# Performance work log

Hardware: AMD Instinct MI355X
Metric: run time of the kernel (lower is better)

## Reference

```python
import jax, jax.numpy as jnp
import numpy as np
from functools import partial

S, N, G2, R, E, IN, OUT = 32, 400, 16, 128, 64, 2, 5


def setup_inputs() -> dict:
    key = jax.random.key(0)
    ks = jax.random.split(key, 16)
    sc = lambda *sh: 1.0 / np.sqrt(sh[-1] if len(sh) > 1 else sh[0])
    return {
        "input_data": jax.random.normal(ks[0], (S, N, IN), jnp.float32),
        "grids": jax.random.uniform(ks[1], (S, N, N, G2), jnp.float32) * (jax.random.uniform(ks[2], (S, N, N, G2)) < 0.05),  # mostly-sparse grid masks
        "hidden_states": jax.random.normal(ks[3], (N, R), jnp.float32) * 0.1,
        "cell_states": jax.random.normal(ks[4], (N, R), jnp.float32) * 0.1,
        "W_in": jax.random.normal(ks[5], (IN, E), jnp.float32) * 0.5,
        "b_in": jax.random.normal(ks[6], (E,), jnp.float32) * 0.1,
        "W_t": jax.random.normal(ks[7], (G2 * R, E), jnp.float32) / np.sqrt(G2 * R),
        "b_t": jax.random.normal(ks[8], (E,), jnp.float32) * 0.1,
        "W_ih": jax.random.normal(ks[9], (4 * R, 2 * E), jnp.float32) / np.sqrt(2 * E),
        "b_ih": jax.random.normal(ks[10], (4 * R,), jnp.float32) * 0.1,
        "W_hh": jax.random.normal(ks[11], (4 * R, R), jnp.float32) / np.sqrt(R),
        "b_hh": jax.random.normal(ks[12], (4 * R,), jnp.float32) * 0.1,
        "W_out": jax.random.normal(ks[13], (R, OUT), jnp.float32) / np.sqrt(R),
        "b_out": jax.random.normal(ks[14], (OUT,), jnp.float32) * 0.1,
    }


def reference(input_data, grids, hidden_states, cell_states, W_in, b_in, W_t, b_t,
              W_ih, b_ih, W_hh, b_hh, W_out, b_out):
    n = hidden_states.shape[0]

    def step(carry, frame):
        h, c = carry
        x_f, grid_f = frame  # [N,2], [N,N,G2]
        # social tensor: for each node, grid[node].T @ hidden  -> [N, G2, R]
        social = jnp.einsum('nmg,mr->ngr', grid_f, h).reshape(n, -1)
        input_emb = jax.nn.relu(x_f @ W_in + b_in)          # dropout = identity (eval)
        tensor_emb = jax.nn.relu(social @ W_t + b_t)
        z = jnp.concatenate([input_emb, tensor_emb], axis=1)  # [N, 2E]
        gates = z @ W_ih.T + b_ih + h @ W_hh.T + b_hh         # [N, 4R]
        i, f, g, o = jnp.split(gates, 4, axis=1)              # torch LSTMCell gate order
        c_new = jax.nn.sigmoid(f) * c + jax.nn.sigmoid(i) * jnp.tanh(g)
        h_new = jax.nn.sigmoid(o) * jnp.tanh(c_new)
        out = h_new @ W_out + b_out
        return (h_new, c_new), out

    (h_fin, c_fin), outputs = jax.lax.scan(step, (hidden_states, cell_states), (input_data, grids))
    return outputs, h_fin, c_fin  # outputs: [S, N, output_size]
```

## Files before the change

kernel.cpp:

```cpp
#include <hip/hip_runtime.h>
#include <hip/hip_bf16.h>
#include <cstdint>

#define S_   32
#define N_   400
#define G2_  16
#define R_   128
#define E_   64
#define KDIM (N_*G2_)
#define COLS 1536
#define CAP  448
#define NB   200
#define NT   512
#define BAR_OFF 27131904

__device__ __forceinline__ float sigmoidf_(float x) { return 1.0f / (1.0f + __expf(-x)); }

__device__ __forceinline__ void ast4(float* p, float v) {
    __hip_atomic_store((unsigned*)p, __float_as_uint(v),
                       __ATOMIC_RELAXED, __HIP_MEMORY_SCOPE_AGENT);
}
__device__ __forceinline__ void ast_u32(uint32_t* p, uint32_t v) {
    __hip_atomic_store(p, v, __ATOMIC_RELAXED, __HIP_MEMORY_SCOPE_AGENT);
}
__device__ __forceinline__ uint32_t ald_u32(const uint32_t* p) {
    return __hip_atomic_load(p, __ATOMIC_RELAXED, __HIP_MEMORY_SCOPE_AGENT);
}
__device__ __forceinline__ float bfext(uint32_t u, int hi) {
    return __uint_as_float(hi ? (u & 0xffff0000u) : (u << 16));
}
__device__ __forceinline__ uint32_t bf16rne(float f) {
    uint32_t b = __float_as_uint(f);
    b += 0x7fffu + ((b >> 16) & 1u);
    return b >> 16;
}

__device__ void gsync(unsigned* slots, unsigned* flag, unsigned ep)
{
    __syncthreads();
    const int b = blockIdx.x, t = threadIdx.x;
    if (b == 0) {
        if (t >= 1 && t < NB) {
            while (__hip_atomic_load(&slots[t], __ATOMIC_RELAXED,
                                     __HIP_MEMORY_SCOPE_AGENT) < ep)
                __builtin_amdgcn_s_sleep(1);
        }
        __syncthreads();
        if (t == 0)
            __hip_atomic_store(flag, ep, __ATOMIC_RELAXED,
                               __HIP_MEMORY_SCOPE_AGENT);
    } else {
        if (t == 0) {
            __hip_atomic_store(&slots[b], ep, __ATOMIC_RELAXED,
                               __HIP_MEMORY_SCOPE_AGENT);
            while (__hip_atomic_load(flag, __ATOMIC_RELAXED,
                                     __HIP_MEMORY_SCOPE_AGENT) < ep)
                __builtin_amdgcn_s_sleep(1);
        }
        __syncthreads();
    }
}

__global__ __launch_bounds__(256) void k_compact(
    const float* __restrict__ grids, uint32_t* __restrict__ pairs,
    int* __restrict__ counts)
{
    int wave = (blockIdx.x << 2) | (threadIdx.x >> 6);
    int lane = threadIdx.x & 63;
    for (int rr = 0; rr < 2; ++rr) {
        int row = wave*2 + rr;
        const float* src = grids + (size_t)row * KDIM;
        uint32_t*    dst = pairs + (size_t)row * CAP;
        int cnt = 0;
        for (int chunk = 0; chunk < KDIM; chunk += 64) {
            int idx = chunk + lane;
            float v = src[idx];
            bool nz = (v != 0.0f);
            unsigned long long mask = __ballot(nz);
            if (mask) {
                if (nz) {
                    int off = __popcll(mask & ((1ull << lane) - 1ull));
                    int pos = cnt + off;
                    if (pos < CAP)
                        dst[pos] = ((uint32_t)idx << 16) | bf16rne(v);
                }
                cnt += __popcll(mask);
            }
        }
        if (lane == 0) counts[row] = (cnt < CAP) ? cnt : CAP;
    }
}

struct FusedArgs {
    const float* x;
    const float* W_in;  const float* b_in;  const float* b_t;
    const float* W_t;   const float* W_hh;  const float* W_ih;
    const float* b_ih;  const float* b_hh;
    const float* h0;    const float* c0;
    const float* W_out; const float* b_out;
    float* WC; float* WihT;
    uint16_t* HG0; uint16_t* HG1;
    const uint32_t* pairs; const int* counts;
    float* out;
    unsigned* slots; unsigned* flag;
};

__device__ __forceinline__ void hg_update(
    const FusedArgs& a, uint16_t* HGn, int n0, int t,
    const float hb[2][128])
{
    if (t >= 256) return;
    float acc[3][2][2] = {};
    #pragma unroll 4
    for (int r = 0; r < 128; ++r) {
        float h0v = hb[0][r], h1v = hb[1][r];
        const float* wr = a.WC + (size_t)r*COLS;
        #pragma unroll
        for (int k = 0; k < 3; ++k) {
            int c = 2*(t + k*256);
            float w0 = wr[c], w1 = wr[c+1];
            acc[k][0][0] += w0*h0v; acc[k][0][1] += w0*h1v;
            acc[k][1][0] += w1*h0v; acc[k][1][1] += w1*h1v;
        }
    }
    #pragma unroll
    for (int k = 0; k < 3; ++k) {
        int c = 2*(t + k*256);
        #pragma unroll
        for (int row = 0; row < 2; ++row) {
            uint32_t d = bf16rne(acc[k][0][row]) | (bf16rne(acc[k][1][row]) << 16);
            ast_u32((uint32_t*)(HGn + (size_t)(n0+row)*COLS + c), d);
        }
    }
}

__global__ __launch_bounds__(512) void k_fused(FusedArgs a)
{
    const int b = blockIdx.x, t = threadIdx.x;
    const int w = t >> 6, lane = t & 63;
    const int n0 = b << 1;
    unsigned ep = 0;

    __shared__ float tp_part[8][64];
    __shared__ float z[2][128];
    __shared__ float gl[2][512];
    __shared__ float hb[2][128];
    __shared__ float cl[2][128];

    for (int i = b*NT + t; i < 128*COLS + 128*512; i += NB*NT) {
        if (i < 128*COLS) {
            int r = i / COLS, col = i - r*COLS;
            float v;
            if (col < 1024) { int g = col >> 6, e = col & 63; v = a.W_t[(g*128 + r)*64 + e]; }
            else            { int j = col - 1024;             v = a.W_hh[j*128 + r]; }
            ast4(&a.WC[i], v);
        } else {
            int i2 = i - 128*COLS;
            ast4(&a.WihT[i2], a.W_ih[(i2 & 511)*128 + (i2 >> 9)]);
        }
    }
    if (t < 256) {
        int qn = t >> 7, r = t & 127;
        hb[qn][r] = a.h0[(n0 + qn)*R_ + r];
        cl[qn][r] = a.c0[(n0 + qn)*R_ + r];
    }
    gsync(a.slots, a.flag, ++ep);
    hg_update(a, a.HG0, n0, t, hb);
    gsync(a.slots, a.flag, ++ep);

    float bias_j = a.b_ih[t] + a.b_hh[t];
    float bt_e = 0, win0 = 0, win1 = 0, bin_e = 0;
    if (t < 128) {
        int e = t & 63;
        bt_e = a.b_t[e]; win0 = a.W_in[e]; win1 = a.W_in[64 + e]; bin_e = a.b_in[e];
    }

    for (int s = 0; s < S_; ++s) {
        const uint16_t* HGc = (s & 1) ? a.HG1 : a.HG0;
        uint16_t*       HGn = (s & 1) ? a.HG0 : a.HG1;

        {
            int qn = w >> 2, qq = w & 3;
            int row = s*N_ + n0 + qn;
            int cnt = a.counts[row];
            const uint32_t* P = a.pairs + (size_t)row * CAP;
            float acc[16];
            #pragma unroll
            for (int u = 0; u < 16; ++u) acc[u] = 0.0f;
            int nb16 = cnt >> 4;
            int lbase = lane & ~1, lodd = lane & 1;
            for (int bi = qq; bi < nb16; bi += 4) {
                const uint4* q4 = reinterpret_cast<const uint4*>(P + (bi << 4));
                uint4 qa = q4[0], qb = q4[1], qc = q4[2], qd = q4[3];
                uint32_t qs[16] = {qa.x,qa.y,qa.z,qa.w, qb.x,qb.y,qb.z,qb.w,
                                   qc.x,qc.y,qc.z,qc.w, qd.x,qd.y,qd.z,qd.w};
                float hv[16];
                #pragma unroll
                for (int u = 0; u < 16; ++u) {
                    const uint32_t* ap = (const uint32_t*)
                        (HGc + (size_t)(qs[u] >> 20)*COLS + ((qs[u] >> 16) & 15u)*64 + lbase);
                    hv[u] = bfext(ald_u32(ap), lodd);
                }
                #pragma unroll
                for (int u = 0; u < 16; ++u)
                    acc[u] += __uint_as_float(qs[u] << 16) * hv[u];
            }
            if (qq == 3) {
                for (int p = nb16 << 4; p < cnt; ++p) {
                    uint32_t q = P[p];
                    const uint32_t* ap = (const uint32_t*)
                        (HGc + (size_t)(q >> 20)*COLS + ((q >> 16) & 15u)*64 + lbase);
                    acc[0] += __uint_as_float(q << 16) * bfext(ald_u32(ap), lodd);
                }
            }
            #pragma unroll
            for (int u = 8; u < 16; ++u) acc[u - 8] += acc[u];
            #pragma unroll
            for (int u = 4; u < 8; ++u) acc[u - 4] += acc[u];
            tp_part[w][lane] = (acc[0] + acc[1]) + (acc[2] + acc[3]);
        }
        __syncthreads();

        if (t < 128) {
            int qn = t >> 6, e = t & 63;
            int row = s*N_ + n0 + qn;
            float tp = (tp_part[4*qn][e] + tp_part[4*qn+1][e])
                     + (tp_part[4*qn+2][e] + tp_part[4*qn+3][e]);
            z[qn][64 + e] = fmaxf(tp + bt_e, 0.0f);
            float x0 = a.x[row*2 + 0], x1 = a.x[row*2 + 1];
            z[qn][e] = fmaxf(x0*win0 + x1*win1 + bin_e, 0.0f);
        }
        __syncthreads();

        {
            float g0 = 0, g1 = 0;
            #pragma unroll 8
            for (int e = 0; e < 128; ++e) {
                float wv = a.WihT[e*512 + t];
                g0 += z[0][e] * wv;
                g1 += z[1][e] * wv;
            }
            int gb = 1024 + (t & ~1), godd = t & 1;
            uint32_t u0 = ald_u32((const uint32_t*)(HGc + (size_t)n0*COLS + gb));
            uint32_t u1 = ald_u32((const uint32_t*)(HGc + (size_t)(n0+1)*COLS + gb));
            gl[0][t] = g0 + bias_j + bfext(u0, godd);
            gl[1][t] = g1 + bias_j + bfext(u1, godd);
        }
        __syncthreads();

        if (t < 256) {
            int qn = t >> 7, r = t & 127;
            float gi = gl[qn][r], gf = gl[qn][128 + r];
            float gg = gl[qn][256 + r], go = gl[qn][384 + r];
            float cn = sigmoidf_(gf)*cl[qn][r] + sigmoidf_(gi)*tanhf(gg);
            float hn = sigmoidf_(go)*tanhf(cn);
            cl[qn][r] = cn;
            hb[qn][r] = hn;
            if (s == S_ - 1) {
                int n = n0 + qn;
                a.out[S_*N_*5 + n*R_ + r]          = hn;
                a.out[S_*N_*5 + N_*R_ + n*R_ + r]  = cn;
            }
        }
        __syncthreads();

        if (s < S_ - 1) hg_update(a, HGn, n0, t, hb);
        if (t >= 480 && t < 490) {
            int tp = t - 480;
            int qn = tp / 5, o = tp - (tp/5)*5;
            float av = a.b_out[o];
            for (int r = 0; r < 128; ++r) av += hb[qn][r] * a.W_out[r*5 + o];
            a.out[(s*N_ + n0 + qn)*5 + o] = av;
        }
        if (s < S_ - 1) gsync(a.slots, a.flag, ++ep);
    }
}

__global__ __launch_bounds__(256) void k_prep(
    const float* __restrict__ W_t, const float* __restrict__ W_hh,
    const float* __restrict__ W_ih, const float* __restrict__ h0,
    const float* __restrict__ c0,
    float* __restrict__ WC, float* __restrict__ WihT,
    float* __restrict__ h, float* __restrict__ c)
{
    const int total = 128*COLS + 128*512 + 2*N_*R_;
    for (int idx = blockIdx.x*256 + threadIdx.x; idx < total; idx += gridDim.x*256) {
        int i = idx;
        if (i < 128*COLS) {
            int r = i / COLS, col = i - r*COLS;
            float v;
            if (col < 1024) { int g = col >> 6, e = col & 63; v = W_t[(g*128 + r)*64 + e]; }
            else            { int j = col - 1024;             v = W_hh[j*128 + r]; }
            WC[i] = v;
        } else if (i < 128*COLS + 128*512) {
            i -= 128*COLS;
            int e = i / 512, j = i - e*512;
            WihT[i] = W_ih[j*128 + e];
        } else {
            i -= 128*COLS + 128*512;
            if (i < N_*R_) h[i] = h0[i];
            else           c[i - N_*R_] = c0[i - N_*R_];
        }
    }
}

__global__ __launch_bounds__(256) void k_hg(
    const float* __restrict__ h, const float* __restrict__ WC,
    float* __restrict__ HG)
{
    __shared__ float hs[8][128];
    int rt = blockIdx.x / 6, ct = blockIdx.x - rt*6;
    int rowbase = rt * 8, colbase = ct * 256;
    #pragma unroll
    for (int k = 0; k < 4; ++k) {
        int i = k*256 + threadIdx.x;
        hs[i >> 7][i & 127] = h[(rowbase + (i >> 7))*R_ + (i & 127)];
    }
    __syncthreads();
    float acc[8] = {0,0,0,0,0,0,0,0};
    int col = colbase + threadIdx.x;
    const float* wcp = WC + col;
    #pragma unroll 4
    for (int r = 0; r < 128; ++r) {
        float wv = wcp[r * COLS];
        #pragma unroll
        for (int i = 0; i < 8; ++i) acc[i] += hs[i][r] * wv;
    }
    #pragma unroll
    for (int i = 0; i < 8; ++i) HG[(rowbase + i)*COLS + col] = acc[i];
}

__global__ __launch_bounds__(256) void k_step(
    int s,
    const float* __restrict__ x,
    const float* __restrict__ W_in, const float* __restrict__ b_in,
    const float* __restrict__ b_t,
    const float* __restrict__ WihT, const float* __restrict__ b_ih,
    const float* __restrict__ b_hh,
    const float* __restrict__ HG,
    const uint32_t* __restrict__ pairs, const int* __restrict__ counts,
    float* __restrict__ h, float* __restrict__ c,
    const float* __restrict__ W_out, const float* __restrict__ b_out,
    float* __restrict__ out, int last)
{
    __shared__ float z[4][128];
    __shared__ float gl[4][512];
    __shared__ float hb[4][128];

    int w = threadIdx.x >> 6, lane = threadIdx.x & 63;
    int n = (blockIdx.x << 2) | w;
    int row = s * N_ + n;

    int cnt = counts[row];
    const uint32_t* P = pairs + (size_t)row * CAP;
    float acc[8] = {0,0,0,0,0,0,0,0};
    int p = 0;
    for (; p + 8 <= cnt; p += 8) {
        uint4 qa = *reinterpret_cast<const uint4*>(P + p);
        uint4 qb = *reinterpret_cast<const uint4*>(P + p + 4);
        uint32_t qs[8] = {qa.x, qa.y, qa.z, qa.w, qb.x, qb.y, qb.z, qb.w};
        #pragma unroll
        for (int u = 0; u < 8; ++u) {
            uint32_t q = qs[u];
            acc[u] += __uint_as_float(q << 16) *
                      HG[(q >> 20)*COLS + ((q >> 16) & 15u)*64 + lane];
        }
    }
    for (; p < cnt; ++p) {
        uint32_t q = P[p];
        acc[0] += __uint_as_float(q << 16) *
                  HG[(q >> 20)*COLS + ((q >> 16) & 15u)*64 + lane];
    }
    float tp = ((acc[0]+acc[1]) + (acc[2]+acc[3])) + ((acc[4]+acc[5]) + (acc[6]+acc[7]));

    z[w][64 + lane] = fmaxf(tp + b_t[lane], 0.0f);
    float x0 = x[row*2 + 0], x1 = x[row*2 + 1];
    z[w][lane] = fmaxf(x0*W_in[lane] + x1*W_in[64 + lane] + b_in[lane], 0.0f);
    __syncthreads();

    int j0 = threadIdx.x, j1 = threadIdx.x + 256;
    float g0[4] = {0,0,0,0}, g1[4] = {0,0,0,0};
    for (int e = 0; e < 128; ++e) {
        float w0 = WihT[e*512 + j0], w1 = WihT[e*512 + j1];
        #pragma unroll
        for (int q = 0; q < 4; ++q) {
            float zv = z[q][e];
            g0[q] += zv * w0;
            g1[q] += zv * w1;
        }
    }
    float bi0 = b_ih[j0] + b_hh[j0], bi1 = b_ih[j1] + b_hh[j1];
    #pragma unroll
    for (int q = 0; q < 4; ++q) {
        int nq = (blockIdx.x << 2) | q;
        gl[q][j0] = g0[q] + bi0 + HG[nq*COLS + 1024 + j0];
        gl[q][j1] = g1[q] + bi1 + HG[nq*COLS + 1024 + j1];
    }
    __syncthreads();

    #pragma unroll
    for (int rep = 0; rep < 2; ++rep) {
        int t = rep*256 + threadIdx.x;
        int q = t >> 7, r = t & 127;
        int nq = (blockIdx.x << 2) | q;
        float gi = gl[q][r], gf = gl[q][128 + r], gg = gl[q][256 + r], go = gl[q][384 + r];
        float cold = c[nq*R_ + r];
        float cn = sigmoidf_(gf)*cold + sigmoidf_(gi)*tanhf(gg);
        float hn = sigmoidf_(go)*tanhf(cn);
        c[nq*R_ + r] = cn;
        h[nq*R_ + r] = hn;
        hb[q][r] = hn;
        if (last) {
            out[S_*N_*5 + nq*R_ + r]            = hn;
            out[S_*N_*5 + N_*R_ + nq*R_ + r]    = cn;
        }
    }
    __syncthreads();

    if (threadIdx.x < 20) {
        int q = threadIdx.x / 5, o = threadIdx.x - (threadIdx.x / 5)*5;
        int nq = (blockIdx.x << 2) | q;
        float a = b_out[o];
        for (int r = 0; r < 128; ++r) a += hb[q][r] * W_out[r*5 + o];
        out[(s*N_ + nq)*5 + o] = a;
    }
}

extern "C" void kernel_launch(void* const* d_in, const int* in_sizes, int n_in,
                              void* d_out, int out_size, void* d_ws, size_t ws_size,
                              hipStream_t stream)
{
    const float* input_data = (const float*)d_in[0];
    const float* grids      = (const float*)d_in[1];
    const float* h0         = (const float*)d_in[2];
    const float* c0         = (const float*)d_in[3];
    const float* W_in       = (const float*)d_in[4];
    const float* b_in       = (const float*)d_in[5];
    const float* W_t        = (const float*)d_in[6];
    const float* b_t        = (const float*)d_in[7];
    const float* W_ih       = (const float*)d_in[8];
    const float* b_ih       = (const float*)d_in[9];
    const float* W_hh       = (const float*)d_in[10];
    const float* b_hh       = (const float*)d_in[11];
    const float* W_out      = (const float*)d_in[12];
    const float* b_out      = (const float*)d_in[13];
    float* out = (float*)d_out;

    char* ws = (char*)d_ws;
    float*    WC     = (float*)(ws + 0);
    float*    WihT   = (float*)(ws + 786432);
    uint16_t* HG0    = (uint16_t*)(ws + 1048576);
    uint16_t* HG1    = (uint16_t*)(ws + 2277376);
    float*    h      = (float*)(ws + 3506176);
    float*    c      = (float*)(ws + 3710976);
    int*      counts = (int*)  (ws + 3915776);
    uint32_t* pairs  = (uint32_t*)(ws + 4194304);
    float*    HGf    = (float*)(ws + 1048576);
    unsigned* slots  = (unsigned*)(ws + BAR_OFF);
    unsigned* flag   = (unsigned*)(ws + BAR_OFF + 1024);

    hipMemsetAsync(ws + BAR_OFF, 0, 2048, stream);
    k_compact<<<dim3(1600), dim3(256), 0, stream>>>(grids, pairs, counts);

    FusedArgs fa;
    fa.x = input_data; fa.W_in = W_in; fa.b_in = b_in; fa.b_t = b_t;
    fa.W_t = W_t; fa.W_hh = W_hh; fa.W_ih = W_ih;
    fa.b_ih = b_ih; fa.b_hh = b_hh;
    fa.h0 = h0; fa.c0 = c0; fa.W_out = W_out; fa.b_out = b_out;
    fa.WC = WC; fa.WihT = WihT; fa.HG0 = HG0; fa.HG1 = HG1;
    fa.pairs = pairs; fa.counts = counts; fa.out = out;
    fa.slots = slots; fa.flag = flag;

    void* kargs[] = { (void*)&fa };
    hipError_t err = hipLaunchCooperativeKernel((void*)k_fused, dim3(NB), dim3(NT),
                                                kargs, 0, stream);
    if (err != hipSuccess) {
        k_prep<<<dim3(512), dim3(256), 0, stream>>>(W_t, W_hh, W_ih, h0, c0, WC, WihT, h, c);
        k_hg<<<dim3(300), dim3(256), 0, stream>>>(h, WC, HGf);
        for (int s = 0; s < S_; ++s) {
            k_step<<<dim3(100), dim3(256), 0, stream>>>(
                s, input_data, W_in, b_in, b_t, WihT, b_ih, b_hh, HGf, pairs, counts,
                h, c, W_out, b_out, out, (int)(s == S_ - 1));
            if (s < S_ - 1)
                k_hg<<<dim3(300), dim3(256), 0, stream>>>(h, WC, HGf);
        }
    }
}
```

Before: 968.3 us.

## Store recurrent weights as packed bf16 and use all-to-all grid barrier

The combined W_t/W_hh weight matrix and the transposed W_ih are now converted once to packed bf16 pairs instead of fp32, which halves the bytes each block streams per timestep in hg_update and the gate matvec. The grid barrier changes from a master-block gather/broadcast to a flat scheme: every block publishes its epoch to a strided slot and polls all the others directly, which removes one round of latency. The trade-offs are lower weight precision and more polling traffic on the slot array.

```diff
diff --git a/kernel.cpp b/kernel.cpp
--- a/kernel.cpp
+++ b/kernel.cpp
@@ -16,10 +16,6 @@
 
 __device__ __forceinline__ float sigmoidf_(float x) { return 1.0f / (1.0f + __expf(-x)); }
 
-__device__ __forceinline__ void ast4(float* p, float v) {
-    __hip_atomic_store((unsigned*)p, __float_as_uint(v),
-                       __ATOMIC_RELAXED, __HIP_MEMORY_SCOPE_AGENT);
-}
 __device__ __forceinline__ void ast_u32(uint32_t* p, uint32_t v) {
     __hip_atomic_store(p, v, __ATOMIC_RELAXED, __HIP_MEMORY_SCOPE_AGENT);
 }
@@ -35,30 +31,19 @@
     return b >> 16;
 }
 
-__device__ void gsync(unsigned* slots, unsigned* flag, unsigned ep)
-{
-    __syncthreads();
-    const int b = blockIdx.x, t = threadIdx.x;
-    if (b == 0) {
-        if (t >= 1 && t < NB) {
-            while (__hip_atomic_load(&slots[t], __ATOMIC_RELAXED,
-                                     __HIP_MEMORY_SCOPE_AGENT) < ep)
-                __builtin_amdgcn_s_sleep(1);
-        }
-        __syncthreads();
-        if (t == 0)
-            __hip_atomic_store(flag, ep, __ATOMIC_RELAXED,
-                               __HIP_MEMORY_SCOPE_AGENT);
-    } else {
-        if (t == 0) {
-            __hip_atomic_store(&slots[b], ep, __ATOMIC_RELAXED,
-                               __HIP_MEMORY_SCOPE_AGENT);
-            while (__hip_atomic_load(flag, __ATOMIC_RELAXED,
-                                     __HIP_MEMORY_SCOPE_AGENT) < ep)
-                __builtin_amdgcn_s_sleep(1);
-        }
-        __syncthreads();
-    }
+__device__ void gsync(unsigned* slots, unsigned ep)
+{
+    __syncthreads();
+    const int t = threadIdx.x;
+    if (t == 0)
+        __hip_atomic_store(&slots[blockIdx.x << 1], ep,
+                           __ATOMIC_RELAXED, __HIP_MEMORY_SCOPE_AGENT);
+    if (t < NB) {
+        while (__hip_atomic_load(&slots[t << 1], __ATOMIC_RELAXED,
+                                 __HIP_MEMORY_SCOPE_AGENT) < ep)
+            __builtin_amdgcn_s_sleep(2);
+    }
+    __syncthreads();
 }
 
 __global__ __launch_bounds__(256) void k_compact(
@@ -98,15 +83,16 @@
     const float* b_ih;  const float* b_hh;
     const float* h0;    const float* c0;
     const float* W_out; const float* b_out;
-    float* WC; float* WihT;
+    uint32_t* WCh;
+    uint32_t* WihTh;
     uint16_t* HG0; uint16_t* HG1;
     const uint32_t* pairs; const int* counts;
     float* out;
-    unsigned* slots; unsigned* flag;
+    unsigned* slots;
 };
 
 __device__ __forceinline__ void hg_update(
-    const FusedArgs& a, uint16_t* HGn, int n0, int t,
+    const uint32_t* __restrict__ WCh, uint16_t* HGn, int n0, int t,
     const float hb[2][128])
 {
     if (t >= 256) return;
@@ -114,18 +100,18 @@
     #pragma unroll 4
     for (int r = 0; r < 128; ++r) {
         float h0v = hb[0][r], h1v = hb[1][r];
-        const float* wr = a.WC + (size_t)r*COLS;
+        const uint32_t* wr = WCh + r*768;
         #pragma unroll
         for (int k = 0; k < 3; ++k) {
-            int c = 2*(t + k*256);
-            float w0 = wr[c], w1 = wr[c+1];
+            uint32_t wp = wr[t + (k << 8)];
+            float w0 = bfext(wp, 0), w1 = bfext(wp, 1);
             acc[k][0][0] += w0*h0v; acc[k][0][1] += w0*h1v;
             acc[k][1][0] += w1*h0v; acc[k][1][1] += w1*h1v;
         }
     }
     #pragma unroll
     for (int k = 0; k < 3; ++k) {
-        int c = 2*(t + k*256);
+        int c = 2*(t + (k << 8));
         #pragma unroll
         for (int row = 0; row < 2; ++row) {
             uint32_t d = bf16rne(acc[k][0][row]) | (bf16rne(acc[k][1][row]) << 16);
@@ -147,16 +133,27 @@
     __shared__ float hb[2][128];
     __shared__ float cl[2][128];
 
-    for (int i = b*NT + t; i < 128*COLS + 128*512; i += NB*NT) {
-        if (i < 128*COLS) {
-            int r = i / COLS, col = i - r*COLS;
-            float v;
-            if (col < 1024) { int g = col >> 6, e = col & 63; v = a.W_t[(g*128 + r)*64 + e]; }
-            else            { int j = col - 1024;             v = a.W_hh[j*128 + r]; }
-            ast4(&a.WC[i], v);
+    for (int i = b*NT + t; i < 128*768 + 64*512; i += NB*NT) {
+        if (i < 128*768) {
+            int r = i / 768, cp = i - r*768;
+            int c0 = cp * 2;
+            float v0, v1;
+            if (c0 < 1024) {
+                int g = c0 >> 6, e = c0 & 63;
+                v0 = a.W_t[(g*128 + r)*64 + e];
+                v1 = a.W_t[(g*128 + r)*64 + e + 1];
+            } else {
+                int j = c0 - 1024;
+                v0 = a.W_hh[j*128 + r];
+                v1 = a.W_hh[(j+1)*128 + r];
+            }
+            ast_u32(&a.WCh[i], bf16rne(v0) | (bf16rne(v1) << 16));
         } else {
-            int i2 = i - 128*COLS;
-            ast4(&a.WihT[i2], a.W_ih[(i2 & 511)*128 + (i2 >> 9)]);
+            int i2 = i - 128*768;
+            int e2 = i2 >> 9, j = i2 & 511;
+            float v0 = a.W_ih[j*128 + 2*e2];
+            float v1 = a.W_ih[j*128 + 2*e2 + 1];
+            ast_u32(&a.WihTh[i2], bf16rne(v0) | (bf16rne(v1) << 16));
         }
     }
     if (t < 256) {
@@ -164,9 +161,9 @@
         hb[qn][r] = a.h0[(n0 + qn)*R_ + r];
         cl[qn][r] = a.c0[(n0 + qn)*R_ + r];
     }
-    gsync(a.slots, a.flag, ++ep);
-    hg_update(a, a.HG0, n0, t, hb);
-    gsync(a.slots, a.flag, ++ep);
+    gsync(a.slots, ++ep);
+    hg_update(a.WCh, a.HG0, n0, t, hb);
+    gsync(a.slots, ++ep);
 
     float bias_j = a.b_ih[t] + a.b_hh[t];
     float bt_e = 0, win0 = 0, win1 = 0, bin_e = 0;
@@ -235,10 +232,11 @@
         {
             float g0 = 0, g1 = 0;
             #pragma unroll 8
-            for (int e = 0; e < 128; ++e) {
-                float wv = a.WihT[e*512 + t];
-                g0 += z[0][e] * wv;
-                g1 += z[1][e] * wv;
+            for (int e2 = 0; e2 < 64; ++e2) {
+                uint32_t wp = a.WihTh[(e2 << 9) + t];
+                float w0 = bfext(wp, 0), w1 = bfext(wp, 1);
+                g0 += z[0][2*e2]*w0 + z[0][2*e2+1]*w1;
+                g1 += z[1][2*e2]*w0 + z[1][2*e2+1]*w1;
             }
             int gb = 1024 + (t & ~1), godd = t & 1;
             uint32_t u0 = ald_u32((const uint32_t*)(HGc + (size_t)n0*COLS + gb));
@@ -264,7 +262,7 @@
         }
         __syncthreads();
 
-        if (s < S_ - 1) hg_update(a, HGn, n0, t, hb);
+        if (s < S_ - 1) hg_update(a.WCh, HGn, n0, t, hb);
         if (t >= 480 && t < 490) {
             int tp = t - 480;
             int qn = tp / 5, o = tp - (tp/5)*5;
@@ -272,7 +270,7 @@
             for (int r = 0; r < 128; ++r) av += hb[qn][r] * a.W_out[r*5 + o];
             a.out[(s*N_ + n0 + qn)*5 + o] = av;
         }
-        if (s < S_ - 1) gsync(a.slots, a.flag, ++ep);
+        if (s < S_ - 1) gsync(a.slots, ++ep);
     }
 }
 
@@ -447,17 +445,18 @@
     float* out = (float*)d_out;
 
     char* ws = (char*)d_ws;
-    float*    WC     = (float*)(ws + 0);
-    float*    WihT   = (float*)(ws + 786432);
-    uint16_t* HG0    = (uint16_t*)(ws + 1048576);
-    uint16_t* HG1    = (uint16_t*)(ws + 2277376);
+    uint32_t* WCh    = (uint32_t*)(ws + 0);
+    uint32_t* WihTh  = (uint32_t*)(ws + 393216);
+    uint16_t* HG0    = (uint16_t*)(ws + 524288);
+    uint16_t* HG1    = (uint16_t*)(ws + 1753088);
+    float*    WCf    = (float*)(ws + 0);
+    float*    WihTf  = (float*)(ws + 786432);
+    float*    HGf    = (float*)(ws + 1048576);
     float*    h      = (float*)(ws + 3506176);
     float*    c      = (float*)(ws + 3710976);
     int*      counts = (int*)  (ws + 3915776);
     uint32_t* pairs  = (uint32_t*)(ws + 4194304);
-    float*    HGf    = (float*)(ws + 1048576);
     unsigned* slots  = (unsigned*)(ws + BAR_OFF);
-    unsigned* flag   = (unsigned*)(ws + BAR_OFF + 1024);
 
     hipMemsetAsync(ws + BAR_OFF, 0, 2048, stream);
     k_compact<<<dim3(1600), dim3(256), 0, stream>>>(grids, pairs, counts);
@@ -467,22 +466,22 @@
     fa.W_t = W_t; fa.W_hh = W_hh; fa.W_ih = W_ih;
     fa.b_ih = b_ih; fa.b_hh = b_hh;
     fa.h0 = h0; fa.c0 = c0; fa.W_out = W_out; fa.b_out = b_out;
-    fa.WC = WC; fa.WihT = WihT; fa.HG0 = HG0; fa.HG1 = HG1;
+    fa.WCh = WCh; fa.WihTh = WihTh; fa.HG0 = HG0; fa.HG1 = HG1;
     fa.pairs = pairs; fa.counts = counts; fa.out = out;
-    fa.slots = slots; fa.flag = flag;
+    fa.slots = slots;
 
     void* kargs[] = { (void*)&fa };
     hipError_t err = hipLaunchCooperativeKernel((void*)k_fused, dim3(NB), dim3(NT),
                                                 kargs, 0, stream);
     if (err != hipSuccess) {
-        k_prep<<<dim3(512), dim3(256), 0, stream>>>(W_t, W_hh, W_ih, h0, c0, WC, WihT, h, c);
-        k_hg<<<dim3(300), dim3(256), 0, stream>>>(h, WC, HGf);
+        k_prep<<<dim3(512), dim3(256), 0, stream>>>(W_t, W_hh, W_ih, h0, c0, WCf, WihTf, h, c);
+        k_hg<<<dim3(300), dim3(256), 0, stream>>>(h, WCf, HGf);
         for (int s = 0; s < S_; ++s) {
             k_step<<<dim3(100), dim3(256), 0, stream>>>(
-                s, input_data, W_in, b_in, b_t, WihT, b_ih, b_hh, HGf, pairs, counts,
+                s, input_data, W_in, b_in, b_t, WihTf, b_ih, b_hh, HGf, pairs, counts,
                 h, c, W_out, b_out, out, (int)(s == S_ - 1));
             if (s < S_ - 1)
-                k_hg<<<dim3(300), dim3(256), 0, stream>>>(h, WC, HGf);
-        }
-    }
-}
+                k_hg<<<dim3(300), dim3(256), 0, stream>>>(h, WCf, HGf);
+        }
+    }
+}
```

Result: faster. 919.2 us (median of 5 runs) (-5.1%).
